# Kernel optimization log

Measured on AMD Instinct MI355X. Metric: run time of the kernel, lower is better.

Reference implementation:

```python
import jax, jax.numpy as jnp
import numpy as np

B, T, C, H = 2, 2048, 1024, 16
D = C // H  # head dim = 64


def setup_inputs() -> dict:
    key = jax.random.key(0)
    ks = jax.random.split(key, 5)
    s = 0.02
    return {
        "x": jax.random.normal(ks[0], (B, T, C), dtype=jnp.float32),
        "c_attn_w": jax.random.normal(ks[1], (C, 3 * C), dtype=jnp.float32) * s,
        "c_attn_b": jax.random.normal(ks[2], (3 * C,), dtype=jnp.float32) * s,
        "c_proj_w": jax.random.normal(ks[3], (C, C), dtype=jnp.float32) * s,
        "c_proj_b": jax.random.normal(ks[4], (C,), dtype=jnp.float32) * s,
    }


def reference(x, c_attn_w, c_attn_b, c_proj_w, c_proj_b):
    b, t, c = x.shape
    # GPT-2 Conv1D: x @ W + b
    qkv = x @ c_attn_w + c_attn_b                      # [B,T,3C]
    q, k, v = jnp.split(qkv, 3, axis=-1)
    # [B,H,T,D]
    q = q.reshape(b, t, H, D).transpose(0, 2, 1, 3)
    k = k.reshape(b, t, H, D).transpose(0, 2, 1, 3)
    v = v.reshape(b, t, H, D).transpose(0, 2, 1, 3)
    scale = 1.0 / jnp.sqrt(jnp.float32(D))
    scores = jnp.einsum("bhqd,bhkd->bhqk", q, k) * scale  # [B,H,T,T]
    causal = jnp.tril(jnp.ones((t, t), dtype=bool))
    scores = jnp.where(causal, scores, jnp.float32(-jnp.inf))
    attn = jax.nn.softmax(scores, axis=-1)
    # drop_rate = 0.0 -> dropout is identity
    y = jnp.einsum("bhqk,bhkd->bhqd", attn, v)          # [B,H,T,D]
    y = y.transpose(0, 2, 1, 3).reshape(b, t, c)
    return y @ c_proj_w + c_proj_b
```

## Files before the change

kernel.cpp:

```cpp
#include <hip/hip_runtime.h>

#define B_ 2
#define T_ 2048
#define C_ 1024
#define H_ 16
#define D_ 64
#define M_ (B_ * T_)
#define NQKV_ (3 * C_)

typedef unsigned short us16;
typedef short bf16x8 __attribute__((ext_vector_type(8)));
typedef float f32x4 __attribute__((ext_vector_type(4)));

__device__ __forceinline__ f32x4 mfma16(bf16x8 a, bf16x8 b, f32x4 c) {
    return __builtin_amdgcn_mfma_f32_16x16x32_bf16(a, b, c, 0, 0, 0);
}

__device__ __forceinline__ us16 f2bf(float f) {
    union { float f; unsigned int u; } v; v.f = f;
    unsigned int r = v.u + 0x7fffu + ((v.u >> 16) & 1u);
    return (us16)(r >> 16);
}

__device__ __forceinline__ unsigned int cvt_pk_bf16(float lo, float hi) {
    unsigned int r;
    asm("v_cvt_pk_bf16_f32 %0, %1, %2" : "=v"(r) : "v"(lo), "v"(hi));
    return r;
}

__device__ __forceinline__ void gl_lds16(const us16* g, us16* l) {
    __builtin_amdgcn_global_load_lds(
        (const __attribute__((address_space(1))) void*)g,
        (__attribute__((address_space(3))) void*)l,
        16, 0, 0);
}

__global__ __launch_bounds__(256) void cvt_bf16(
    const float* __restrict__ in, us16* __restrict__ out, int n8)
{
    const int i = blockIdx.x * blockDim.x + threadIdx.x;
    if (i >= n8) return;
    const float4 a = ((const float4*)in)[2 * i];
    const float4 b = ((const float4*)in)[2 * i + 1];
    ushort4 lo = { f2bf(a.x), f2bf(a.y), f2bf(a.z), f2bf(a.w) };
    ushort4 hi = { f2bf(b.x), f2bf(b.y), f2bf(b.z), f2bf(b.w) };
    ((ushort4*)out)[2 * i] = lo;
    ((ushort4*)out)[2 * i + 1] = hi;
}

__global__ __launch_bounds__(256) void transpose_cvt(
    const float* __restrict__ W, us16* __restrict__ Wt, int K, int N)
{
    __shared__ float tile[32][33];
    const int n0 = blockIdx.x * 32, k0 = blockIdx.y * 32;
    const int t = threadIdx.x;
    {
        const int k = t >> 3, n4 = (t & 7) * 4;
        const float4 v = *(const float4*)(W + (size_t)(k0 + k) * N + n0 + n4);
        tile[k][n4 + 0] = v.x; tile[k][n4 + 1] = v.y;
        tile[k][n4 + 2] = v.z; tile[k][n4 + 3] = v.w;
    }
    __syncthreads();
    {
        const int n = t >> 3, k4 = (t & 7) * 4;
        ushort4 o = { f2bf(tile[k4 + 0][n]), f2bf(tile[k4 + 1][n]),
                      f2bf(tile[k4 + 2][n]), f2bf(tile[k4 + 3][n]) };
        *(ushort4*)(Wt + (size_t)(n0 + n) * K + k0 + k4) = o;
    }
}

__global__ __launch_bounds__(256) void gemm_bf16(
    const us16* __restrict__ A, const us16* __restrict__ Bt,
    const float* __restrict__ bias, void* __restrict__ Cout,
    int M, int N, int K, int out_bf16)
{
    __shared__ __align__(16) us16 smem[128 * 136];
    us16* sA = smem;
    us16* sB = smem + 128 * 64;

    const int tid = threadIdx.x;
    const int lane = tid & 63, wave = tid >> 6;
    const int wr = wave >> 1, wc = wave & 1;
    const int cq = lane & 15, quad = lane >> 4;
    const int m0 = blockIdx.y * 128, n0 = blockIdx.x * 128;

    const int srow  = lane >> 3;
    const int sgran = (lane & 7) ^ srow;
    const int scol  = sgran * 8;

    f32x4 acc[4][4];
    #pragma unroll
    for (int i = 0; i < 4; ++i)
        #pragma unroll
        for (int j = 0; j < 4; ++j)
            acc[i][j] = (f32x4){0.f, 0.f, 0.f, 0.f};

    for (int k0 = 0; k0 < K; k0 += 64) {
        #pragma unroll
        for (int p = 0; p < 4; ++p) {
            const int r = p * 32 + wave * 8;
            gl_lds16(A  + (size_t)(m0 + r + srow) * K + k0 + scol, sA + r * 64);
            gl_lds16(Bt + (size_t)(n0 + r + srow) * K + k0 + scol, sB + r * 64);
        }
        __syncthreads();

        #pragma unroll
        for (int kk = 0; kk < 64; kk += 32) {
            const int koS = (((kk >> 3) + quad) ^ (cq & 7)) << 3;
            bf16x8 af[4], bfg[4];
            #pragma unroll
            for (int i = 0; i < 4; ++i) {
                af[i]  = *(const bf16x8*)(sA + (wr * 64 + i * 16 + cq) * 64 + koS);
                bfg[i] = *(const bf16x8*)(sB + (wc * 64 + i * 16 + cq) * 64 + koS);
            }
            #pragma unroll
            for (int mi = 0; mi < 4; ++mi)
                #pragma unroll
                for (int ni = 0; ni < 4; ++ni)
                    acc[mi][ni] = mfma16(af[mi], bfg[ni], acc[mi][ni]);
        }
        __syncthreads();
    }

    if (out_bf16) {
        us16* Cs = smem;
        #pragma unroll
        for (int mi = 0; mi < 4; ++mi)
            #pragma unroll
            for (int ni = 0; ni < 4; ++ni) {
                const int n = n0 + wc * 64 + ni * 16 + cq;
                const float bv = bias[n];
                #pragma unroll
                for (int r = 0; r < 4; ++r)
                    Cs[(wr * 64 + mi * 16 + quad * 4 + r) * 136 +
                       wc * 64 + ni * 16 + cq] = f2bf(acc[mi][ni][r] + bv);
            }
        __syncthreads();
        us16* Co = (us16*)Cout;
        #pragma unroll
        for (int p = 0; p < 8; ++p) {
            const int chunk = p * 256 + tid;
            const int r = chunk >> 4, c = (chunk & 15) * 8;
            *(uint4*)(Co + (size_t)(m0 + r) * N + n0 + c) =
                *(const uint4*)(Cs + r * 136 + c);
        }
    } else {
        float* Co = (float*)Cout;
        #pragma unroll
        for (int mi = 0; mi < 4; ++mi)
            #pragma unroll
            for (int ni = 0; ni < 4; ++ni) {
                const int n = n0 + wc * 64 + ni * 16 + cq;
                const float bv = bias[n];
                #pragma unroll
                for (int r = 0; r < 4; ++r)
                    Co[(size_t)(m0 + wr * 64 + mi * 16 + quad * 4 + r) * N + n] =
                        acc[mi][ni][r] + bv;
            }
    }
}

__global__ __launch_bounds__(256) void attn_mfma(
    const us16* __restrict__ qkv, us16* __restrict__ y)
{
    __shared__ __align__(16) us16 Ks[64][72];
    __shared__ __align__(16) us16 Vt[64][72];
    __shared__ __align__(16) us16 Ps[64][72];

    const int tid = threadIdx.x;
    const int lane = tid & 63, wave = tid >> 6;
    const int cq = lane & 15, quad = lane >> 4;
    const int bh = blockIdx.x;
    const int qt = (int)gridDim.y - 1 - (int)blockIdx.y;
    const int b = bh >> 4, h = bh & 15;

    const us16* base = qkv + (size_t)b * T_ * NQKV_ + h * D_;

    bf16x8 qf[2];
    {
        const us16* qrow = base + (size_t)(qt * 64 + wave * 16 + cq) * NQKV_;
        qf[0] = *(const bf16x8*)(qrow + quad * 8);
        qf[1] = *(const bf16x8*)(qrow + 32 + quad * 8);
    }

    f32x4 ot[4];
    #pragma unroll
    for (int j = 0; j < 4; ++j) ot[j] = (f32x4){0.f, 0.f, 0.f, 0.f};
    f32x4 os = (f32x4){0.f, 0.f, 0.f, 0.f};

    const bf16x8 onesf = (bf16x8){16256, 16256, 16256, 16256,
                                  16256, 16256, 16256, 16256};

    const float SCL = 0.125f * 1.44269504089f;
    const float SH  = -3.0f * 1.44269504089f;

    const int t2 = tid & 31, dc = tid >> 5;

    for (int kt = 0; kt <= qt; ++kt) {
        __syncthreads();
        #pragma unroll
        for (int p = 0; p < 2; ++p) {
            const int chunk = p * 256 + tid;
            const int r = chunk >> 3, c8 = (chunk & 7) * 8;
            const uint4 v = *(const uint4*)(base + (size_t)(kt * 64 + r) * NQKV_ + C_ + c8);
            *(uint4*)(&Ks[r][c8]) = v;
        }
        {
            const us16* vp = base + (size_t)(kt * 64 + 2 * t2) * NQKV_ + 2 * C_ + dc * 8;
            const uint4 u0 = *(const uint4*)vp;
            const uint4 u1 = *(const uint4*)(vp + NQKV_);
            const us16* p0 = (const us16*)&u0;
            const us16* p1 = (const us16*)&u1;
            #pragma unroll
            for (int j = 0; j < 8; ++j) {
                const unsigned int packed =
                    (unsigned int)p0[j] | ((unsigned int)p1[j] << 16);
                *(unsigned int*)(&Vt[dc * 8 + j][2 * t2]) = packed;
            }
        }
        __syncthreads();

        f32x4 s[4];
        #pragma unroll
        for (int j = 0; j < 4; ++j) {
            const bf16x8 kf0 = *(const bf16x8*)(&Ks[j * 16 + cq][quad * 8]);
            const bf16x8 kf1 = *(const bf16x8*)(&Ks[j * 16 + cq][32 + quad * 8]);
            f32x4 t = (f32x4){0.f, 0.f, 0.f, 0.f};
            t = mfma16(qf[0], kf0, t);
            t = mfma16(qf[1], kf1, t);
            s[j] = t;
        }

        float p[4][4];
        if (kt == qt) {
            const int qloc = wave * 16 + quad * 4;
            #pragma unroll
            for (int j = 0; j < 4; ++j) {
                const int kloc = j * 16 + cq;
                #pragma unroll
                for (int r = 0; r < 4; ++r) {
                    const float e = exp2f(fmaf(s[j][r], SCL, SH));
                    p[j][r] = (kloc > qloc + r) ? 0.f : e;
                }
            }
        } else {
            #pragma unroll
            for (int j = 0; j < 4; ++j)
                #pragma unroll
                for (int r = 0; r < 4; ++r)
                    p[j][r] = exp2f(fmaf(s[j][r], SCL, SH));
        }

        #pragma unroll
        for (int j = 0; j < 4; ++j) {
            const unsigned int pk01 = cvt_pk_bf16(p[j][0], p[j][1]);
            const unsigned int pk23 = cvt_pk_bf16(p[j][2], p[j][3]);
            us16* pp = &Ps[wave * 16 + quad * 4][j * 16 + cq];
            pp[0]       = (us16)pk01;
            pp[72]      = (us16)(pk01 >> 16);
            pp[2 * 72]  = (us16)pk23;
            pp[3 * 72]  = (us16)(pk23 >> 16);
        }

        const bf16x8 pf0 = *(const bf16x8*)(&Ps[wave * 16 + cq][quad * 8]);
        const bf16x8 pf1 = *(const bf16x8*)(&Ps[wave * 16 + cq][32 + quad * 8]);

        os = mfma16(onesf, pf0, os);
        os = mfma16(onesf, pf1, os);
        #pragma unroll
        for (int dt = 0; dt < 4; ++dt) {
            const bf16x8 vf0 = *(const bf16x8*)(&Vt[dt * 16 + cq][quad * 8]);
            const bf16x8 vf1 = *(const bf16x8*)(&Vt[dt * 16 + cq][32 + quad * 8]);
            ot[dt] = mfma16(vf0, pf0, ot[dt]);
            ot[dt] = mfma16(vf1, pf1, ot[dt]);
        }
    }

    const float inv = 1.0f / os[0];
    const int row = qt * 64 + wave * 16 + cq;
    us16* yp = y + (size_t)(b * T_ + row) * C_ + h * D_ + quad * 4;
    #pragma unroll
    for (int dt = 0; dt < 4; ++dt) {
        ushort4 ov = { f2bf(ot[dt][0] * inv), f2bf(ot[dt][1] * inv),
                       f2bf(ot[dt][2] * inv), f2bf(ot[dt][3] * inv) };
        *(ushort4*)(yp + dt * 16) = ov;
    }
}

extern "C" void kernel_launch(void* const* d_in, const int* in_sizes, int n_in,
                              void* d_out, int out_size, void* d_ws, size_t ws_size,
                              hipStream_t stream)
{
    const float* x  = (const float*)d_in[0];
    const float* aw = (const float*)d_in[1];
    const float* ab = (const float*)d_in[2];
    const float* pw = (const float*)d_in[3];
    const float* pb = (const float*)d_in[4];
    float* out = (float*)d_out;

    us16* xb   = (us16*)d_ws;
    us16* awT  = xb  + (size_t)M_ * C_;
    us16* pwT  = awT + (size_t)NQKV_ * C_;
    us16* qkvb = pwT + (size_t)C_ * C_;
    us16* yb   = qkvb + (size_t)M_ * NQKV_;

    cvt_bf16<<<(M_ * C_ / 8 + 255) / 256, 256, 0, stream>>>(x, xb, M_ * C_ / 8);
    transpose_cvt<<<dim3(NQKV_ / 32, C_ / 32), 256, 0, stream>>>(aw, awT, C_, NQKV_);
    transpose_cvt<<<dim3(C_ / 32, C_ / 32), 256, 0, stream>>>(pw, pwT, C_, C_);

    gemm_bf16<<<dim3(NQKV_ / 128, M_ / 128), 256, 0, stream>>>(
        xb, awT, ab, qkvb, M_, NQKV_, C_, 1);

    attn_mfma<<<dim3(B_ * H_, T_ / 64), 256, 0, stream>>>(qkvb, yb);

    gemm_bf16<<<dim3(C_ / 128, M_ / 128), 256, 0, stream>>>(
        yb, pwT, pb, out, M_, C_, C_, 0);
}
```

Measured before the change: 215.4 us.

## Process two query tiles per attention block to share K/V tile loads

Each attention workgroup now handles 128 query rows, as two 64-row sub-tiles, instead of 64, and the grid is halved. Every K/V tile staged into shared memory is reused for both sub-tiles, which halves global K/V traffic and the transpose/sync overhead per query row. In exchange, causal masking is now evaluated on every iteration, the first sub-tile does one fully masked wasted tile, and register pressure roughly doubles for the accumulators. The smaller grid also leaves fewer workgroups to balance the causal work across CUs.

Result: slower. 223.8 us (+3.9%).

```diff
diff --git a/kernel.cpp b/kernel.cpp
--- a/kernel.cpp
+++ b/kernel.cpp
@@ -171,22 +171,30 @@
     const int lane = tid & 63, wave = tid >> 6;
     const int cq = lane & 15, quad = lane >> 4;
     const int bh = blockIdx.x;
-    const int qt = (int)gridDim.y - 1 - (int)blockIdx.y;
+    const int g = (int)gridDim.y - 1 - (int)blockIdx.y;
     const int b = bh >> 4, h = bh & 15;
 
     const us16* base = qkv + (size_t)b * T_ * NQKV_ + h * D_;
 
-    bf16x8 qf[2];
-    {
-        const us16* qrow = base + (size_t)(qt * 64 + wave * 16 + cq) * NQKV_;
-        qf[0] = *(const bf16x8*)(qrow + quad * 8);
-        qf[1] = *(const bf16x8*)(qrow + 32 + quad * 8);
-    }
-
-    f32x4 ot[4];
+    const int qrA = g * 128 + wave * 16 + cq;
+    bf16x8 qfA[2], qfB[2];
+    {
+        const us16* qa = base + (size_t)qrA * NQKV_;
+        qfA[0] = *(const bf16x8*)(qa + quad * 8);
+        qfA[1] = *(const bf16x8*)(qa + 32 + quad * 8);
+        const us16* qb = qa + (size_t)64 * NQKV_;
+        qfB[0] = *(const bf16x8*)(qb + quad * 8);
+        qfB[1] = *(const bf16x8*)(qb + 32 + quad * 8);
+    }
+
+    f32x4 otA[4], otB[4];
     #pragma unroll
-    for (int j = 0; j < 4; ++j) ot[j] = (f32x4){0.f, 0.f, 0.f, 0.f};
-    f32x4 os = (f32x4){0.f, 0.f, 0.f, 0.f};
+    for (int j = 0; j < 4; ++j) {
+        otA[j] = (f32x4){0.f, 0.f, 0.f, 0.f};
+        otB[j] = (f32x4){0.f, 0.f, 0.f, 0.f};
+    }
+    f32x4 osA = (f32x4){0.f, 0.f, 0.f, 0.f};
+    f32x4 osB = (f32x4){0.f, 0.f, 0.f, 0.f};
 
     const bf16x8 onesf = (bf16x8){16256, 16256, 16256, 16256,
                                   16256, 16256, 16256, 16256};
@@ -195,8 +203,11 @@
     const float SH  = -3.0f * 1.44269504089f;
 
     const int t2 = tid & 31, dc = tid >> 5;
-
-    for (int kt = 0; kt <= qt; ++kt) {
+    const int kmax = 2 * g + 1;
+    const int qgA = g * 128 + wave * 16 + quad * 4;
+    const int qgB = qgA + 64;
+
+    for (int kt = 0; kt <= kmax; ++kt) {
         __syncthreads();
         #pragma unroll
         for (int p = 0; p < 2; ++p) {
@@ -220,70 +231,108 @@
         }
         __syncthreads();
 
-        f32x4 s[4];
+        f32x4 s0[4], s1[4];
         #pragma unroll
         for (int j = 0; j < 4; ++j) {
             const bf16x8 kf0 = *(const bf16x8*)(&Ks[j * 16 + cq][quad * 8]);
             const bf16x8 kf1 = *(const bf16x8*)(&Ks[j * 16 + cq][32 + quad * 8]);
-            f32x4 t = (f32x4){0.f, 0.f, 0.f, 0.f};
-            t = mfma16(qf[0], kf0, t);
-            t = mfma16(qf[1], kf1, t);
-            s[j] = t;
-        }
-
-        float p[4][4];
-        if (kt == qt) {
-            const int qloc = wave * 16 + quad * 4;
+            f32x4 ta = (f32x4){0.f, 0.f, 0.f, 0.f};
+            ta = mfma16(qfA[0], kf0, ta);
+            ta = mfma16(qfA[1], kf1, ta);
+            s0[j] = ta;
+            f32x4 tb = (f32x4){0.f, 0.f, 0.f, 0.f};
+            tb = mfma16(qfB[0], kf0, tb);
+            tb = mfma16(qfB[1], kf1, tb);
+            s1[j] = tb;
+        }
+
+        {
+            float p[4][4];
             #pragma unroll
             for (int j = 0; j < 4; ++j) {
-                const int kloc = j * 16 + cq;
+                const int kg = kt * 64 + j * 16 + cq;
                 #pragma unroll
                 for (int r = 0; r < 4; ++r) {
-                    const float e = exp2f(fmaf(s[j][r], SCL, SH));
-                    p[j][r] = (kloc > qloc + r) ? 0.f : e;
+                    const float e = exp2f(fmaf(s0[j][r], SCL, SH));
+                    p[j][r] = (kg > qgA + r) ? 0.f : e;
                 }
             }
-        } else {
-            #pragma unroll
-            for (int j = 0; j < 4; ++j)
-                #pragma unroll
-                for (int r = 0; r < 4; ++r)
-                    p[j][r] = exp2f(fmaf(s[j][r], SCL, SH));
-        }
-
-        #pragma unroll
-        for (int j = 0; j < 4; ++j) {
-            const unsigned int pk01 = cvt_pk_bf16(p[j][0], p[j][1]);
-            const unsigned int pk23 = cvt_pk_bf16(p[j][2], p[j][3]);
-            us16* pp = &Ps[wave * 16 + quad * 4][j * 16 + cq];
-            pp[0]       = (us16)pk01;
-            pp[72]      = (us16)(pk01 >> 16);
-            pp[2 * 72]  = (us16)pk23;
-            pp[3 * 72]  = (us16)(pk23 >> 16);
-        }
-
-        const bf16x8 pf0 = *(const bf16x8*)(&Ps[wave * 16 + cq][quad * 8]);
-        const bf16x8 pf1 = *(const bf16x8*)(&Ps[wave * 16 + cq][32 + quad * 8]);
-
-        os = mfma16(onesf, pf0, os);
-        os = mfma16(onesf, pf1, os);
+            #pragma unroll
+            for (int j = 0; j < 4; ++j) {
+                const unsigned int pk01 = cvt_pk_bf16(p[j][0], p[j][1]);
+                const unsigned int pk23 = cvt_pk_bf16(p[j][2], p[j][3]);
+                us16* pp = &Ps[wave * 16 + quad * 4][j * 16 + cq];
+                pp[0]       = (us16)pk01;
+                pp[72]      = (us16)(pk01 >> 16);
+                pp[2 * 72]  = (us16)pk23;
+                pp[3 * 72]  = (us16)(pk23 >> 16);
+            }
+            const bf16x8 pf0 = *(const bf16x8*)(&Ps[wave * 16 + cq][quad * 8]);
+            const bf16x8 pf1 = *(const bf16x8*)(&Ps[wave * 16 + cq][32 + quad * 8]);
+            osA = mfma16(onesf, pf0, osA);
+            osA = mfma16(onesf, pf1, osA);
+            #pragma unroll
+            for (int dt = 0; dt < 4; ++dt) {
+                const bf16x8 vf0 = *(const bf16x8*)(&Vt[dt * 16 + cq][quad * 8]);
+                const bf16x8 vf1 = *(const bf16x8*)(&Vt[dt * 16 + cq][32 + quad * 8]);
+                otA[dt] = mfma16(vf0, pf0, otA[dt]);
+                otA[dt] = mfma16(vf1, pf1, otA[dt]);
+            }
+        }
+        {
+            float p[4][4];
+            #pragma unroll
+            for (int j = 0; j < 4; ++j) {
+                const int kg = kt * 64 + j * 16 + cq;
+                #pragma unroll
+                for (int r = 0; r < 4; ++r) {
+                    const float e = exp2f(fmaf(s1[j][r], SCL, SH));
+                    p[j][r] = (kg > qgB + r) ? 0.f : e;
+                }
+            }
+            #pragma unroll
+            for (int j = 0; j < 4; ++j) {
+                const unsigned int pk01 = cvt_pk_bf16(p[j][0], p[j][1]);
+                const unsigned int pk23 = cvt_pk_bf16(p[j][2], p[j][3]);
+                us16* pp = &Ps[wave * 16 + quad * 4][j * 16 + cq];
+                pp[0]       = (us16)pk01;
+                pp[72]      = (us16)(pk01 >> 16);
+                pp[2 * 72]  = (us16)pk23;
+                pp[3 * 72]  = (us16)(pk23 >> 16);
+            }
+            const bf16x8 pf0 = *(const bf16x8*)(&Ps[wave * 16 + cq][quad * 8]);
+            const bf16x8 pf1 = *(const bf16x8*)(&Ps[wave * 16 + cq][32 + quad * 8]);
+            osB = mfma16(onesf, pf0, osB);
+            osB = mfma16(onesf, pf1, osB);
+            #pragma unroll
+            for (int dt = 0; dt < 4; ++dt) {
+                const bf16x8 vf0 = *(const bf16x8*)(&Vt[dt * 16 + cq][quad * 8]);
+                const bf16x8 vf1 = *(const bf16x8*)(&Vt[dt * 16 + cq][32 + quad * 8]);
+                otB[dt] = mfma16(vf0, pf0, otB[dt]);
+                otB[dt] = mfma16(vf1, pf1, otB[dt]);
+            }
+        }
+    }
+
+    {
+        const float inv = 1.0f / osA[0];
+        us16* yp = y + (size_t)(b * T_ + qrA) * C_ + h * D_ + quad * 4;
         #pragma unroll
         for (int dt = 0; dt < 4; ++dt) {
-            const bf16x8 vf0 = *(const bf16x8*)(&Vt[dt * 16 + cq][quad * 8]);
-            const bf16x8 vf1 = *(const bf16x8*)(&Vt[dt * 16 + cq][32 + quad * 8]);
-            ot[dt] = mfma16(vf0, pf0, ot[dt]);
-            ot[dt] = mfma16(vf1, pf1, ot[dt]);
-        }
-    }
-
-    const float inv = 1.0f / os[0];
-    const int row = qt * 64 + wave * 16 + cq;
-    us16* yp = y + (size_t)(b * T_ + row) * C_ + h * D_ + quad * 4;
-    #pragma unroll
-    for (int dt = 0; dt < 4; ++dt) {
-        ushort4 ov = { f2bf(ot[dt][0] * inv), f2bf(ot[dt][1] * inv),
-                       f2bf(ot[dt][2] * inv), f2bf(ot[dt][3] * inv) };
-        *(ushort4*)(yp + dt * 16) = ov;
+            ushort4 ov = { f2bf(otA[dt][0] * inv), f2bf(otA[dt][1] * inv),
+                           f2bf(otA[dt][2] * inv), f2bf(otA[dt][3] * inv) };
+            *(ushort4*)(yp + dt * 16) = ov;
+        }
+    }
+    {
+        const float inv = 1.0f / osB[0];
+        us16* yp = y + (size_t)(b * T_ + qrA + 64) * C_ + h * D_ + quad * 4;
+        #pragma unroll
+        for (int dt = 0; dt < 4; ++dt) {
+            ushort4 ov = { f2bf(otB[dt][0] * inv), f2bf(otB[dt][1] * inv),
+                           f2bf(otB[dt][2] * inv), f2bf(otB[dt][3] * inv) };
+            *(ushort4*)(yp + dt * 16) = ov;
+        }
     }
 }
 
@@ -311,7 +360,7 @@
     gemm_bf16<<<dim3(NQKV_ / 128, M_ / 128), 256, 0, stream>>>(
         xb, awT, ab, qkvb, M_, NQKV_, C_, 1);
 
-    attn_mfma<<<dim3(B_ * H_, T_ / 64), 256, 0, stream>>>(qkvb, yb);
+    attn_mfma<<<dim3(B_ * H_, T_ / 128), 256, 0, stream>>>(qkvb, yb);
 
     gemm_bf16<<<dim3(C_ / 128, M_ / 128), 256, 0, stream>>>(
         yb, pwT, pb, out, M_, C_, C_, 0);
```
